# Performance work log

Hardware: AMD Instinct MI355X
Metric: run time of the kernel (lower is better)

## Reference

```python
import jax, jax.numpy as jnp
import numpy as np
import math


def _dct2_mat(N):
    # DCT-II matrix, norm=None convention of torch_dct: X[k] = 2*sum_n x[n]*cos(pi*(2n+1)*k/(2N))
    n = np.arange(N)
    k = n[:, None]
    C = 2.0 * np.cos(np.pi * (2 * n[None, :] + 1) * k / (2 * N))
    return jnp.asarray(C, dtype=jnp.float32)


def setup_inputs() -> dict:
    key = jax.random.key(0)
    k1, k2, k3 = jax.random.split(key, 3)
    B, H, W = 128, 256, 256
    thresh = int(H / (2 * math.sqrt(2)))  # 90
    x = jax.random.normal(k1, (B, 3, H, W), dtype=jnp.float32)
    w = jax.random.normal(k2, (1, thresh), dtype=jnp.float32) * 0.05
    b = jax.random.normal(k3, (1,), dtype=jnp.float32) * 0.05
    return {"x": x, "w": w, "b": b}


def reference(x, w, b):
    B, C, H, W = x.shape
    Ch = _dct2_mat(H)
    Cw = _dct2_mat(W)
    # dct_2d: DCT-II along last two dims
    xd = jnp.einsum('bchw,kw->bchk', x, Cw)
    xd = jnp.einsum('bchk,jh->bcjk', xd, Ch)
    xd = jax.lax.stop_gradient(xd)  # original does x.detach() inside get_fft_feature
    gray = 0.2989 * xd[:, 0] + 0.587 * xd[:, 1] + 0.114 * xd[:, 2]  # [B,H,W]
    F = jnp.fft.fft2(gray, axes=(-2, -1))
    re = F.real + 1e-8  # original adds epsilon to both real and imag parts
    im = F.imag + 1e-8
    mag = jnp.log(jnp.sqrt(re * re + im * im + 1e-10) + 1e-10)
    mag = jnp.fft.fftshift(mag, axes=(-2, -1))  # quadrant-swap `shift` == fftshift for even dims
    # radial binning (static integer radii, as in azimuthalAverage)
    yy, xx = np.indices([H, W])
    r = np.sqrt((xx - H / 2) ** 2 + (yy - W / 2) ** 2).astype(np.int32).ravel()
    nbins = int(r.max()) + 1
    nr = jnp.asarray(np.bincount(r, minlength=nbins).astype(np.float32))
    rj = jnp.asarray(r)
    tbin = jax.vmap(lambda m: jax.ops.segment_sum(m, rj, num_segments=nbins))(mag.reshape(B, -1))
    prof = tbin / (nr + 1e-10)  # [B, nbins]
    prof = prof[:, 1:-2]  # azimuthalAverage returns radial_prof[1:-2]
    mn = jnp.min(prof, axis=1, keepdims=True)
    mx = jnp.max(prof, axis=1, keepdims=True)
    out = (prof - mn) / (mx - mn)
    out = jnp.where(jnp.isnan(out), 0.0, out)
    thresh = w.shape[1]
    feat = out[:, -thresh:]  # [B, thresh]
    return feat @ w.T + b  # [B, 1]
```

## Files before the change

### kernel.cpp

```cpp
#include <hip/hip_runtime.h>
#include <math.h>

#define NBINS 182
#define NB 128

typedef unsigned short u16;
typedef __attribute__((ext_vector_type(8))) short short8;
typedef __attribute__((ext_vector_type(4))) float f32x4;

__device__ __forceinline__ u16 f2bf(float f) {
    union { float f; unsigned u; } v; v.f = f;
    unsigned r = v.u + 0x7FFF + ((v.u >> 16) & 1);
    return (u16)(r >> 16);
}
__device__ __forceinline__ float bf2f(u16 u) {
    union { unsigned u; float f; } v; v.u = ((unsigned)u) << 16;
    return v.f;
}
__device__ __forceinline__ short8 negbf(short8 v) {
    short8 r;
#pragma unroll
    for (int i = 0; i < 8; ++i) r[i] = v[i] ^ (short)0x8000;
    return r;
}

__device__ __forceinline__ int radial_bin(int dx, int dy) {
    int d2 = dx * dx + dy * dy;
    int bin = (int)sqrtf((float)d2);
    while ((bin + 1) * (bin + 1) <= d2) ++bin;
    while (bin * bin > d2) --bin;
    return bin;
}

__global__ __launch_bounds__(256) void prep(const float* __restrict__ x,
                                            u16* __restrict__ G,
                                            float* __restrict__ M_re,
                                            float* __restrict__ M_im,
                                            u16* __restrict__ A1,
                                            float* __restrict__ nrpart,
                                            float* __restrict__ tbin) {
    __shared__ double ctab[1024];
    __shared__ double stab[1024];
    __shared__ float s[NBINS];
    int blk = blockIdx.x;
    int t = threadIdx.x;

    if (blk < 256) {
        for (int i = t; i < 1024; i += 256) {
            double a = 3.14159265358979323846 * (double)i / 512.0;
            ctab[i] = cos(a);
            stab[i] = sin(a);
        }
        __syncthreads();
        int j = blk;
        int w = t;
        double re = 0.0, im = 0.0;
        int tw = 2 * w + 1;
        for (int k = 0; k < 256; ++k) {
            int e = (4 * j * k) & 1023;
            int m = (tw * k) & 1023;
            double cw = 2.0 * ctab[m];
            re += ctab[e] * cw;
            im -= stab[e] * cw;
        }
        M_re[j * 256 + w] = (float)re;
        M_im[j * 256 + w] = (float)im;
        A1[j * 256 + w] = f2bf((float)re);
        A1[(j + 256) * 256 + w] = f2bf((float)im);
    } else if (blk < 512) {
        int i = blk - 256;
        if (t < NBINS) s[t] = 0.0f;
        __syncthreads();
        int bin = radial_bin(t - 128, i - 128);
        atomicAdd(&s[bin], 1.0f);
        __syncthreads();
        if (t < NBINS) nrpart[i * NBINS + t] = s[t];
    } else if (blk < 544) {
        int idx = (blk - 512) * 256 + t;
        for (int i = idx; i < NB * NBINS; i += 32 * 256) tbin[i] = 0.0f;
    } else {
        int tid = (blk - 544) * 256 + t;
        for (int i = tid; i < 2097152; i += 262144) {
            int idx = i * 4;
            int b = idx >> 16;
            int rem = idx & 65535;
            const float* p = x + (size_t)b * 196608 + rem;
            float4 r = *(const float4*)p;
            float4 g = *(const float4*)(p + 65536);
            float4 bl = *(const float4*)(p + 131072);
            float g0 = 0.2989f * r.x + 0.587f * g.x + 0.114f * bl.x;
            float g1 = 0.2989f * r.y + 0.587f * g.y + 0.114f * bl.y;
            float g2 = 0.2989f * r.z + 0.587f * g.z + 0.114f * bl.z;
            float g3 = 0.2989f * r.w + 0.587f * g.w + 0.114f * bl.w;
            uint2 o;
            o.x = (unsigned)f2bf(g0) | ((unsigned)f2bf(g1) << 16);
            o.y = (unsigned)f2bf(g2) | ((unsigned)f2bf(g3) << 16);
            *(uint2*)(G + idx) = o;
        }
    }
}

__global__ __launch_bounds__(256) void s1(const u16* __restrict__ A1,
                                          const u16* __restrict__ G,
                                          u16* __restrict__ Tt_re,
                                          u16* __restrict__ Tt_im) {
    __shared__ u16 As[128 * 40];
    __shared__ u16 Bs[128 * 40];
    int b = blockIdx.z;
    int r0 = blockIdx.y * 128;
    int h0 = blockIdx.x * 128;
    int t = threadIdx.x;
    int lane = t & 63, wv = t >> 6;
    int wr = (wv >> 1) * 64;
    int wc = (wv & 1) * 64;
    int fr = lane & 15;
    int fk = (lane >> 4) << 3;

    f32x4 acc[4][4];
#pragma unroll
    for (int i = 0; i < 4; ++i)
#pragma unroll
        for (int j = 0; j < 4; ++j) acc[i][j] = (f32x4){0.f, 0.f, 0.f, 0.f};

    const u16* Ap = A1 + (size_t)r0 * 256;
    const u16* Gp = G + (size_t)b * 65536 + (size_t)h0 * 256;

    for (int kk = 0; kk < 256; kk += 32) {
#pragma unroll
        for (int c = t; c < 512; c += 256) {
            int row = c >> 2, off = (c & 3) << 3;
            *(uint4*)&As[row * 40 + off] =
                *(const uint4*)(Ap + (size_t)row * 256 + kk + off);
            *(uint4*)&Bs[row * 40 + off] =
                *(const uint4*)(Gp + (size_t)row * 256 + kk + off);
        }
        __syncthreads();
        short8 af[4], bfr[4];
#pragma unroll
        for (int i = 0; i < 4; ++i)
            af[i] = *(const short8*)&As[(wr + i * 16 + fr) * 40 + fk];
#pragma unroll
        for (int j = 0; j < 4; ++j)
            bfr[j] = *(const short8*)&Bs[(wc + j * 16 + fr) * 40 + fk];
#pragma unroll
        for (int i = 0; i < 4; ++i)
#pragma unroll
            for (int j = 0; j < 4; ++j)
                acc[i][j] = __builtin_amdgcn_mfma_f32_16x16x32_bf16(
                    af[i], bfr[j], acc[i][j], 0, 0, 0);
        __syncthreads();
    }

    u16* dst = ((r0 < 256) ? Tt_re : Tt_im) + (size_t)b * 65536
             + (size_t)(r0 & 255) * 256;
    int rq = (lane >> 4) << 2;
#pragma unroll
    for (int i = 0; i < 4; ++i)
#pragma unroll
        for (int j = 0; j < 4; ++j) {
            int col = h0 + wc + j * 16 + fr;
#pragma unroll
            for (int reg = 0; reg < 4; ++reg) {
                int row = wr + i * 16 + rq + reg;
                dst[(size_t)row * 256 + col] = f2bf(acc[i][j][reg]);
            }
        }
}

__global__ __launch_bounds__(256) void s2f(const u16* __restrict__ A1,
                                           const float* __restrict__ M_re,
                                           const u16* __restrict__ Tt_re,
                                           const u16* __restrict__ Tt_im,
                                           float* __restrict__ tbin) {
    __shared__ u16 Ar[64 * 40], Ai[64 * 40], Br[64 * 40], Bi[64 * 40];
    __shared__ float sbins[NBINS];
    __shared__ float sM[256];
    int blk = blockIdx.x;
    int t = threadIdx.x;

    if (blk >= 1024) {
        int b = blk - 1024;
        sM[t] = M_re[128 * 256 + t];
        __syncthreads();
        if (t > 128) return;
        const u16* pr = Tt_re + (size_t)b * 65536 + (size_t)t * 256;
        const u16* pi = Tt_im + (size_t)b * 65536 + (size_t)t * 256;
        float re = 0.0f, im = 0.0f;
        for (int h = 0; h < 256; h += 8) {
            uint4 vr = *(const uint4*)(pr + h);
            uint4 vi = *(const uint4*)(pi + h);
            unsigned wr[4] = {vr.x, vr.y, vr.z, vr.w};
            unsigned wi[4] = {vi.x, vi.y, vi.z, vi.w};
#pragma unroll
            for (int q = 0; q < 4; ++q) {
                re = fmaf(sM[h + 2 * q], bf2f((u16)(wr[q] & 0xffff)), re);
                re = fmaf(sM[h + 2 * q + 1], bf2f((u16)(wr[q] >> 16)), re);
                im = fmaf(sM[h + 2 * q], bf2f((u16)(wi[q] & 0xffff)), im);
                im = fmaf(sM[h + 2 * q + 1], bf2f((u16)(wi[q] >> 16)), im);
            }
        }
        re += 1e-8f; im += 1e-8f;
        float mag = logf(sqrtf(re * re + im * im + 1e-10f) + 1e-10f);
        float wj = (t == 0 || t == 128) ? 1.0f : 2.0f;
        int dx = (t < 128) ? t : t - 256;
        int bin = radial_bin(dx, -128);
        atomicAdd(&tbin[b * NBINS + bin], wj * mag);
        return;
    }

    int b = blk >> 3;
    int u0 = ((blk >> 2) & 1) * 64;
    int j0 = (blk & 3) * 64;
    int lane = t & 63, wv = t >> 6;
    int wu = (wv >> 1) * 32;
    int wj = (wv & 1) * 32;
    int fr = lane & 15;
    int fk = (lane >> 4) << 3;

    for (int i = t; i < NBINS; i += 256) sbins[i] = 0.0f;

    f32x4 accr[2][2], acci[2][2];
#pragma unroll
    for (int i = 0; i < 2; ++i)
#pragma unroll
        for (int j = 0; j < 2; ++j) {
            accr[i][j] = (f32x4){0.f, 0.f, 0.f, 0.f};
            acci[i][j] = (f32x4){0.f, 0.f, 0.f, 0.f};
        }

    const u16* Apr = A1 + (size_t)u0 * 256;
    const u16* Api = A1 + (size_t)(256 + u0) * 256;
    const u16* Tr = Tt_re + (size_t)b * 65536 + (size_t)j0 * 256;
    const u16* Ti = Tt_im + (size_t)b * 65536 + (size_t)j0 * 256;

    int lrow = t >> 2, loff = (t & 3) << 3;

    for (int kk = 0; kk < 256; kk += 32) {
        *(uint4*)&Ar[lrow * 40 + loff] =
            *(const uint4*)(Apr + (size_t)lrow * 256 + kk + loff);
        *(uint4*)&Ai[lrow * 40 + loff] =
            *(const uint4*)(Api + (size_t)lrow * 256 + kk + loff);
        *(uint4*)&Br[lrow * 40 + loff] =
            *(const uint4*)(Tr + (size_t)lrow * 256 + kk + loff);
        *(uint4*)&Bi[lrow * 40 + loff] =
            *(const uint4*)(Ti + (size_t)lrow * 256 + kk + loff);
        __syncthreads();
        short8 arf[2], aif[2], naif[2], brf[2], bif[2];
#pragma unroll
        for (int i = 0; i < 2; ++i) {
            arf[i] = *(const short8*)&Ar[(wu + i * 16 + fr) * 40 + fk];
            aif[i] = *(const short8*)&Ai[(wu + i * 16 + fr) * 40 + fk];
            naif[i] = negbf(aif[i]);
        }
#pragma unroll
        for (int j = 0; j < 2; ++j) {
            brf[j] = *(const short8*)&Br[(wj + j * 16 + fr) * 40 + fk];
            bif[j] = *(const short8*)&Bi[(wj + j * 16 + fr) * 40 + fk];
        }
#pragma unroll
        for (int i = 0; i < 2; ++i)
#pragma unroll
            for (int j = 0; j < 2; ++j) {
                accr[i][j] = __builtin_amdgcn_mfma_f32_16x16x32_bf16(
                    arf[i], brf[j], accr[i][j], 0, 0, 0);
                accr[i][j] = __builtin_amdgcn_mfma_f32_16x16x32_bf16(
                    naif[i], bif[j], accr[i][j], 0, 0, 0);
                acci[i][j] = __builtin_amdgcn_mfma_f32_16x16x32_bf16(
                    arf[i], bif[j], acci[i][j], 0, 0, 0);
                acci[i][j] = __builtin_amdgcn_mfma_f32_16x16x32_bf16(
                    aif[i], brf[j], acci[i][j], 0, 0, 0);
            }
        __syncthreads();
    }

    int rq = (lane >> 4) << 2;
#pragma unroll
    for (int i = 0; i < 2; ++i)
#pragma unroll
        for (int j = 0; j < 2; ++j) {
            int v = j0 + wj + j * 16 + fr;
            int dx = (v < 128) ? v : v - 256;
#pragma unroll
            for (int reg = 0; reg < 4; ++reg) {
                int u = u0 + wu + i * 16 + rq + reg;
                float wrow = (u == 0) ? 1.0f : 2.0f;
                int bin = radial_bin(dx, u);
                float re = accr[i][j][reg] + 1e-8f;
                float im = acci[i][j][reg] + 1e-8f;
                float mag = logf(sqrtf(re * re + im * im + 1e-10f) + 1e-10f);
                atomicAdd(&sbins[bin], wrow * mag);
            }
        }
    __syncthreads();
    for (int i = t; i < NBINS; i += 256)
        atomicAdd(&tbin[b * NBINS + i], sbins[i]);
}

__global__ __launch_bounds__(192) void finalize(const float* __restrict__ tbin,
                                                const float* __restrict__ nrpart,
                                                const float* __restrict__ w,
                                                const float* __restrict__ bias,
                                                float* __restrict__ out) {
    __shared__ float prof[NBINS];
    __shared__ float smn, smx, ssum;
    int b = blockIdx.x;
    int t = threadIdx.x;
    if (t < NBINS) {
        float nr = 0.0f;
        for (int i = 0; i < 256; ++i) nr += nrpart[i * NBINS + t];
        prof[t] = tbin[b * NBINS + t] / (nr + 1e-10f);
    }
    __syncthreads();
    if (t == 0) {
        float mn = prof[1], mx = prof[1];
        for (int i = 2; i <= 179; ++i) {
            float p = prof[i];
            mn = fminf(mn, p);
            mx = fmaxf(mx, p);
        }
        smn = mn; smx = mx; ssum = 0.0f;
    }
    __syncthreads();
    if (t < 90) {
        float denom = smx - smn;
        float v = (prof[90 + t] - smn) / denom;
        if (v != v) v = 0.0f;
        atomicAdd(&ssum, v * w[t]);
    }
    __syncthreads();
    if (t == 0) out[b] = ssum + bias[0];
}

extern "C" void kernel_launch(void* const* d_in, const int* in_sizes, int n_in,
                              void* d_out, int out_size, void* d_ws, size_t ws_size,
                              hipStream_t stream) {
    const float* x = (const float*)d_in[0];
    const float* w = (const float*)d_in[1];
    const float* bias = (const float*)d_in[2];
    float* out = (float*)d_out;

    float* M_re = (float*)d_ws;
    float* M_im = M_re + 65536;
    u16* A1 = (u16*)(M_im + 65536);
    u16* G = A1 + 131072;
    u16* Tt_re = G + (size_t)NB * 65536;
    u16* Tt_im = Tt_re + (size_t)NB * 65536;
    float* tbin = (float*)(Tt_im + (size_t)NB * 65536);
    float* nrpart = tbin + NB * NBINS;

    prep<<<1568, 256, 0, stream>>>(x, G, M_re, M_im, A1, nrpart, tbin);
    s1<<<dim3(2, 4, NB), 256, 0, stream>>>(A1, G, Tt_re, Tt_im);
    s2f<<<1152, 256, 0, stream>>>(A1, M_re, Tt_re, Tt_im, tbin);
    finalize<<<NB, 192, 0, stream>>>(tbin, nrpart, w, bias, out);
}
```

Before: 229.5 us.

## Exploit conjugate symmetry of real-input transform to halve first-stage GEMM

The first matmul stage now computes only rows 0..128 of the complex transform of the real gray image. The second stage reconstructs rows above 128 by mirroring (row 256-j) and flipping the sign of the imaginary part, so the s1 grid shrinks from 4 to 3 row-tiles. A small special block computes the lone row 128, and prep zeroes the matching imaginary row. This roughly halves first-stage MFMA work and Tt writes, at the cost of extra index logic, a sign-flip XOR in s2f loads and an unevenly sized extra block.

```diff
diff --git a/kernel.cpp b/kernel.cpp
--- a/kernel.cpp
+++ b/kernel.cpp
@@ -38,7 +38,8 @@
                                             float* __restrict__ M_im,
                                             u16* __restrict__ A1,
                                             float* __restrict__ nrpart,
-                                            float* __restrict__ tbin) {
+                                            float* __restrict__ tbin,
+                                            u16* __restrict__ Tt_im) {
     __shared__ double ctab[1024];
     __shared__ double stab[1024];
     __shared__ float s[NBINS];
@@ -78,6 +79,10 @@
     } else if (blk < 544) {
         int idx = (blk - 512) * 256 + t;
         for (int i = idx; i < NB * NBINS; i += 32 * 256) tbin[i] = 0.0f;
+        for (int i = idx; i < NB * 128; i += 32 * 256) {
+            int b = i >> 7, off = (i & 127) << 1;
+            *(unsigned*)(Tt_im + (size_t)b * 65536 + 128 * 256 + off) = 0u;
+        }
     } else {
         int tid = (blk - 544) * 256 + t;
         for (int i = tid; i < 2097152; i += 262144) {
@@ -104,12 +109,40 @@
                                           const u16* __restrict__ G,
                                           u16* __restrict__ Tt_re,
                                           u16* __restrict__ Tt_im) {
+    int b = blockIdx.z;
+    int t = threadIdx.x;
+
+    if (blockIdx.y == 2) {
+        int lane = t & 63, wv = t >> 6;
+        int fr = lane & 15;
+        int fk = (lane >> 4) << 3;
+        const u16* Ap = A1 + (size_t)(128 + fr) * 256;
+        const u16* Gb = G + (size_t)b * 65536;
+        int c0 = blockIdx.x * 128 + wv * 32;
+        f32x4 acc[2];
+        acc[0] = (f32x4){0.f, 0.f, 0.f, 0.f};
+        acc[1] = (f32x4){0.f, 0.f, 0.f, 0.f};
+        for (int kk = 0; kk < 256; kk += 32) {
+            short8 af = *(const short8*)(Ap + kk + fk);
+#pragma unroll
+            for (int sub = 0; sub < 2; ++sub) {
+                short8 bfv = *(const short8*)(Gb + (size_t)(c0 + sub * 16 + fr) * 256 + kk + fk);
+                acc[sub] = __builtin_amdgcn_mfma_f32_16x16x32_bf16(
+                    af, bfv, acc[sub], 0, 0, 0);
+            }
+        }
+        if ((lane >> 4) == 0) {
+            size_t base = (size_t)b * 65536 + 128 * 256;
+            Tt_re[base + c0 + lane] = f2bf(acc[0][0]);
+            Tt_re[base + c0 + 16 + lane] = f2bf(acc[1][0]);
+        }
+        return;
+    }
+
     __shared__ u16 As[128 * 40];
     __shared__ u16 Bs[128 * 40];
-    int b = blockIdx.z;
-    int r0 = blockIdx.y * 128;
+    int r0 = blockIdx.y * 256;
     int h0 = blockIdx.x * 128;
-    int t = threadIdx.x;
     int lane = t & 63, wv = t >> 6;
     int wr = (wv >> 1) * 64;
     int wc = (wv & 1) * 64;
@@ -151,8 +184,7 @@
         __syncthreads();
     }
 
-    u16* dst = ((r0 < 256) ? Tt_re : Tt_im) + (size_t)b * 65536
-             + (size_t)(r0 & 255) * 256;
+    u16* dst = ((r0 < 256) ? Tt_re : Tt_im) + (size_t)b * 65536;
     int rq = (lane >> 4) << 2;
 #pragma unroll
     for (int i = 0; i < 4; ++i)
@@ -230,20 +262,23 @@
 
     const u16* Apr = A1 + (size_t)u0 * 256;
     const u16* Api = A1 + (size_t)(256 + u0) * 256;
-    const u16* Tr = Tt_re + (size_t)b * 65536 + (size_t)j0 * 256;
-    const u16* Ti = Tt_im + (size_t)b * 65536 + (size_t)j0 * 256;
 
     int lrow = t >> 2, loff = (t & 3) << 3;
+    int jp = j0 + lrow;
+    int src = (jp <= 128) ? jp : 256 - jp;
+    unsigned imask = (jp > 128) ? 0x80008000u : 0u;
+    const u16* Trs = Tt_re + (size_t)b * 65536 + (size_t)src * 256;
+    const u16* Tis = Tt_im + (size_t)b * 65536 + (size_t)src * 256;
 
     for (int kk = 0; kk < 256; kk += 32) {
         *(uint4*)&Ar[lrow * 40 + loff] =
             *(const uint4*)(Apr + (size_t)lrow * 256 + kk + loff);
         *(uint4*)&Ai[lrow * 40 + loff] =
             *(const uint4*)(Api + (size_t)lrow * 256 + kk + loff);
-        *(uint4*)&Br[lrow * 40 + loff] =
-            *(const uint4*)(Tr + (size_t)lrow * 256 + kk + loff);
-        *(uint4*)&Bi[lrow * 40 + loff] =
-            *(const uint4*)(Ti + (size_t)lrow * 256 + kk + loff);
+        *(uint4*)&Br[lrow * 40 + loff] = *(const uint4*)(Trs + kk + loff);
+        uint4 vi = *(const uint4*)(Tis + kk + loff);
+        vi.x ^= imask; vi.y ^= imask; vi.z ^= imask; vi.w ^= imask;
+        *(uint4*)&Bi[lrow * 40 + loff] = vi;
         __syncthreads();
         short8 arf[2], aif[2], naif[2], brf[2], bif[2];
 #pragma unroll
@@ -348,8 +383,8 @@
     float* tbin = (float*)(Tt_im + (size_t)NB * 65536);
     float* nrpart = tbin + NB * NBINS;
 
-    prep<<<1568, 256, 0, stream>>>(x, G, M_re, M_im, A1, nrpart, tbin);
-    s1<<<dim3(2, 4, NB), 256, 0, stream>>>(A1, G, Tt_re, Tt_im);
+    prep<<<1568, 256, 0, stream>>>(x, G, M_re, M_im, A1, nrpart, tbin, Tt_im);
+    s1<<<dim3(2, 3, NB), 256, 0, stream>>>(A1, G, Tt_re, Tt_im);
     s2f<<<1152, 256, 0, stream>>>(A1, M_re, Tt_re, Tt_im, tbin);
     finalize<<<NB, 192, 0, stream>>>(tbin, nrpart, w, bias, out);
 }
```

Measured after the change: 223.9 us. -2.5%, faster.

## Fuse grayscale into first DFT stage, exploit Hermitian symmetry, merge finalize into s2f

Applied to the files above, without the earlier changes.

The grayscale conversion moves out of prep and into s1, which now reads x directly and builds bf16 tiles in shared memory. This removes the G intermediate buffer and one global round trip. s1 computes only rows 0..128 of the first-stage transform by using conjugate symmetry (real input), and s2f rebuilds rows above 128 by mirroring and sign-flipping the imaginary part. The finalize kernel is folded into s2f through a per-batch completion counter with a threadfence, so the last block for each batch computes the output. This cuts launches and memory traffic but adds atomic-counter synchronization and a more complex indexing scheme.

```diff
diff --git a/kernel.cpp b/kernel.cpp
--- a/kernel.cpp
+++ b/kernel.cpp
@@ -32,13 +32,13 @@
     return bin;
 }
 
-__global__ __launch_bounds__(256) void prep(const float* __restrict__ x,
-                                            u16* __restrict__ G,
-                                            float* __restrict__ M_re,
+__global__ __launch_bounds__(256) void prep(float* __restrict__ M_re,
                                             float* __restrict__ M_im,
                                             u16* __restrict__ A1,
                                             float* __restrict__ nrpart,
-                                            float* __restrict__ tbin) {
+                                            float* __restrict__ tbin,
+                                            u16* __restrict__ Tt_im,
+                                            unsigned* __restrict__ done) {
     __shared__ double ctab[1024];
     __shared__ double stab[1024];
     __shared__ float s[NBINS];
@@ -75,44 +75,31 @@
         atomicAdd(&s[bin], 1.0f);
         __syncthreads();
         if (t < NBINS) nrpart[i * NBINS + t] = s[t];
-    } else if (blk < 544) {
+    } else {
         int idx = (blk - 512) * 256 + t;
-        for (int i = idx; i < NB * NBINS; i += 32 * 256) tbin[i] = 0.0f;
-    } else {
-        int tid = (blk - 544) * 256 + t;
-        for (int i = tid; i < 2097152; i += 262144) {
-            int idx = i * 4;
-            int b = idx >> 16;
-            int rem = idx & 65535;
-            const float* p = x + (size_t)b * 196608 + rem;
-            float4 r = *(const float4*)p;
-            float4 g = *(const float4*)(p + 65536);
-            float4 bl = *(const float4*)(p + 131072);
-            float g0 = 0.2989f * r.x + 0.587f * g.x + 0.114f * bl.x;
-            float g1 = 0.2989f * r.y + 0.587f * g.y + 0.114f * bl.y;
-            float g2 = 0.2989f * r.z + 0.587f * g.z + 0.114f * bl.z;
-            float g3 = 0.2989f * r.w + 0.587f * g.w + 0.114f * bl.w;
-            uint2 o;
-            o.x = (unsigned)f2bf(g0) | ((unsigned)f2bf(g1) << 16);
-            o.y = (unsigned)f2bf(g2) | ((unsigned)f2bf(g3) << 16);
-            *(uint2*)(G + idx) = o;
-        }
-    }
-}
-
-__global__ __launch_bounds__(256) void s1(const u16* __restrict__ A1,
-                                          const u16* __restrict__ G,
+        for (int i = idx; i < NB * NBINS; i += 8192) tbin[i] = 0.0f;
+        for (int i = idx; i < NB * 128; i += 8192) {
+            int bb = i >> 7, off = (i & 127) << 1;
+            *(unsigned*)(Tt_im + (size_t)bb * 65536 + 128 * 256 + off) = 0u;
+        }
+        if (idx < NB) done[idx] = 0u;
+    }
+}
+
+__global__ __launch_bounds__(512) void s1(const u16* __restrict__ A1,
+                                          const float* __restrict__ x,
                                           u16* __restrict__ Tt_re,
                                           u16* __restrict__ Tt_im) {
-    __shared__ u16 As[128 * 40];
+    __shared__ u16 As[272 * 40];
     __shared__ u16 Bs[128 * 40];
     int b = blockIdx.z;
-    int r0 = blockIdx.y * 128;
     int h0 = blockIdx.x * 128;
     int t = threadIdx.x;
     int lane = t & 63, wv = t >> 6;
-    int wr = (wv >> 1) * 64;
-    int wc = (wv & 1) * 64;
+    int w4 = wv & 3;
+    int wr = (w4 >> 1) * 64;
+    int wc = (w4 & 1) * 64;
+    int aOff = (wv >= 4) ? 128 : 0;
     int fr = lane & 15;
     int fk = (lane >> 4) << 3;
 
@@ -121,24 +108,46 @@
     for (int i = 0; i < 4; ++i)
 #pragma unroll
         for (int j = 0; j < 4; ++j) acc[i][j] = (f32x4){0.f, 0.f, 0.f, 0.f};
-
-    const u16* Ap = A1 + (size_t)r0 * 256;
-    const u16* Gp = G + (size_t)b * 65536 + (size_t)h0 * 256;
+    f32x4 acc128 = (f32x4){0.f, 0.f, 0.f, 0.f};
+
+    int srow = t >> 2, swq = (t & 3) << 3;
+    const float* xp = x + (size_t)b * 196608 + (size_t)(h0 + srow) * 256 + swq;
 
     for (int kk = 0; kk < 256; kk += 32) {
-#pragma unroll
-        for (int c = t; c < 512; c += 256) {
+        for (int c = t; c < 1088; c += 512) {
             int row = c >> 2, off = (c & 3) << 3;
+            int src = (row < 128) ? row : ((row < 256) ? row + 128 : row - 128);
             *(uint4*)&As[row * 40 + off] =
-                *(const uint4*)(Ap + (size_t)row * 256 + kk + off);
-            *(uint4*)&Bs[row * 40 + off] =
-                *(const uint4*)(Gp + (size_t)row * 256 + kk + off);
+                *(const uint4*)(A1 + (size_t)src * 256 + kk + off);
+        }
+        {
+            const float* p = xp + kk;
+            float4 ra = *(const float4*)p;
+            float4 rb = *(const float4*)(p + 4);
+            float4 ga = *(const float4*)(p + 65536);
+            float4 gb = *(const float4*)(p + 65540);
+            float4 ba = *(const float4*)(p + 131072);
+            float4 bb = *(const float4*)(p + 131076);
+            float q0 = 0.2989f * ra.x + 0.587f * ga.x + 0.114f * ba.x;
+            float q1 = 0.2989f * ra.y + 0.587f * ga.y + 0.114f * ba.y;
+            float q2 = 0.2989f * ra.z + 0.587f * ga.z + 0.114f * ba.z;
+            float q3 = 0.2989f * ra.w + 0.587f * ga.w + 0.114f * ba.w;
+            float q4 = 0.2989f * rb.x + 0.587f * gb.x + 0.114f * bb.x;
+            float q5 = 0.2989f * rb.y + 0.587f * gb.y + 0.114f * bb.y;
+            float q6 = 0.2989f * rb.z + 0.587f * gb.z + 0.114f * bb.z;
+            float q7 = 0.2989f * rb.w + 0.587f * gb.w + 0.114f * bb.w;
+            uint4 o;
+            o.x = (unsigned)f2bf(q0) | ((unsigned)f2bf(q1) << 16);
+            o.y = (unsigned)f2bf(q2) | ((unsigned)f2bf(q3) << 16);
+            o.z = (unsigned)f2bf(q4) | ((unsigned)f2bf(q5) << 16);
+            o.w = (unsigned)f2bf(q6) | ((unsigned)f2bf(q7) << 16);
+            *(uint4*)&Bs[srow * 40 + swq] = o;
         }
         __syncthreads();
         short8 af[4], bfr[4];
 #pragma unroll
         for (int i = 0; i < 4; ++i)
-            af[i] = *(const short8*)&As[(wr + i * 16 + fr) * 40 + fk];
+            af[i] = *(const short8*)&As[(aOff + wr + i * 16 + fr) * 40 + fk];
 #pragma unroll
         for (int j = 0; j < 4; ++j)
             bfr[j] = *(const short8*)&Bs[(wc + j * 16 + fr) * 40 + fk];
@@ -148,11 +157,16 @@
             for (int j = 0; j < 4; ++j)
                 acc[i][j] = __builtin_amdgcn_mfma_f32_16x16x32_bf16(
                     af[i], bfr[j], acc[i][j], 0, 0, 0);
-        __syncthreads();
-    }
-
-    u16* dst = ((r0 < 256) ? Tt_re : Tt_im) + (size_t)b * 65536
-             + (size_t)(r0 & 255) * 256;
+        {
+            short8 a128 = *(const short8*)&As[(256 + fr) * 40 + fk];
+            short8 b128 = *(const short8*)&Bs[(wv * 16 + fr) * 40 + fk];
+            acc128 = __builtin_amdgcn_mfma_f32_16x16x32_bf16(
+                a128, b128, acc128, 0, 0, 0);
+        }
+        __syncthreads();
+    }
+
+    u16* dst = ((wv < 4) ? Tt_re : Tt_im) + (size_t)b * 65536;
     int rq = (lane >> 4) << 2;
 #pragma unroll
     for (int i = 0; i < 4; ++i)
@@ -165,170 +179,183 @@
                 dst[(size_t)row * 256 + col] = f2bf(acc[i][j][reg]);
             }
         }
+    if ((lane >> 4) == 0)
+        Tt_re[(size_t)b * 65536 + 128 * 256 + h0 + wv * 16 + fr] = f2bf(acc128[0]);
 }
 
 __global__ __launch_bounds__(256) void s2f(const u16* __restrict__ A1,
                                            const float* __restrict__ M_re,
                                            const u16* __restrict__ Tt_re,
                                            const u16* __restrict__ Tt_im,
-                                           float* __restrict__ tbin) {
+                                           float* __restrict__ tbin,
+                                           const float* __restrict__ nrpart,
+                                           const float* __restrict__ wgt,
+                                           const float* __restrict__ bias,
+                                           float* __restrict__ out,
+                                           unsigned* __restrict__ done) {
     __shared__ u16 Ar[64 * 40], Ai[64 * 40], Br[64 * 40], Bi[64 * 40];
     __shared__ float sbins[NBINS];
     __shared__ float sM[256];
+    __shared__ float prof[NBINS];
+    __shared__ float smn, smx, ssum;
+    __shared__ int sOld;
     int blk = blockIdx.x;
     int t = threadIdx.x;
+    int b;
 
     if (blk >= 1024) {
-        int b = blk - 1024;
+        b = blk - 1024;
         sM[t] = M_re[128 * 256 + t];
         __syncthreads();
-        if (t > 128) return;
-        const u16* pr = Tt_re + (size_t)b * 65536 + (size_t)t * 256;
-        const u16* pi = Tt_im + (size_t)b * 65536 + (size_t)t * 256;
-        float re = 0.0f, im = 0.0f;
-        for (int h = 0; h < 256; h += 8) {
-            uint4 vr = *(const uint4*)(pr + h);
-            uint4 vi = *(const uint4*)(pi + h);
-            unsigned wr[4] = {vr.x, vr.y, vr.z, vr.w};
-            unsigned wi[4] = {vi.x, vi.y, vi.z, vi.w};
-#pragma unroll
-            for (int q = 0; q < 4; ++q) {
-                re = fmaf(sM[h + 2 * q], bf2f((u16)(wr[q] & 0xffff)), re);
-                re = fmaf(sM[h + 2 * q + 1], bf2f((u16)(wr[q] >> 16)), re);
-                im = fmaf(sM[h + 2 * q], bf2f((u16)(wi[q] & 0xffff)), im);
-                im = fmaf(sM[h + 2 * q + 1], bf2f((u16)(wi[q] >> 16)), im);
-            }
-        }
-        re += 1e-8f; im += 1e-8f;
-        float mag = logf(sqrtf(re * re + im * im + 1e-10f) + 1e-10f);
-        float wj = (t == 0 || t == 128) ? 1.0f : 2.0f;
-        int dx = (t < 128) ? t : t - 256;
-        int bin = radial_bin(dx, -128);
-        atomicAdd(&tbin[b * NBINS + bin], wj * mag);
-        return;
-    }
-
-    int b = blk >> 3;
-    int u0 = ((blk >> 2) & 1) * 64;
-    int j0 = (blk & 3) * 64;
-    int lane = t & 63, wv = t >> 6;
-    int wu = (wv >> 1) * 32;
-    int wj = (wv & 1) * 32;
-    int fr = lane & 15;
-    int fk = (lane >> 4) << 3;
-
-    for (int i = t; i < NBINS; i += 256) sbins[i] = 0.0f;
-
-    f32x4 accr[2][2], acci[2][2];
-#pragma unroll
-    for (int i = 0; i < 2; ++i)
-#pragma unroll
-        for (int j = 0; j < 2; ++j) {
-            accr[i][j] = (f32x4){0.f, 0.f, 0.f, 0.f};
-            acci[i][j] = (f32x4){0.f, 0.f, 0.f, 0.f};
-        }
-
-    const u16* Apr = A1 + (size_t)u0 * 256;
-    const u16* Api = A1 + (size_t)(256 + u0) * 256;
-    const u16* Tr = Tt_re + (size_t)b * 65536 + (size_t)j0 * 256;
-    const u16* Ti = Tt_im + (size_t)b * 65536 + (size_t)j0 * 256;
-
-    int lrow = t >> 2, loff = (t & 3) << 3;
-
-    for (int kk = 0; kk < 256; kk += 32) {
-        *(uint4*)&Ar[lrow * 40 + loff] =
-            *(const uint4*)(Apr + (size_t)lrow * 256 + kk + loff);
-        *(uint4*)&Ai[lrow * 40 + loff] =
-            *(const uint4*)(Api + (size_t)lrow * 256 + kk + loff);
-        *(uint4*)&Br[lrow * 40 + loff] =
-            *(const uint4*)(Tr + (size_t)lrow * 256 + kk + loff);
-        *(uint4*)&Bi[lrow * 40 + loff] =
-            *(const uint4*)(Ti + (size_t)lrow * 256 + kk + loff);
-        __syncthreads();
-        short8 arf[2], aif[2], naif[2], brf[2], bif[2];
-#pragma unroll
-        for (int i = 0; i < 2; ++i) {
-            arf[i] = *(const short8*)&Ar[(wu + i * 16 + fr) * 40 + fk];
-            aif[i] = *(const short8*)&Ai[(wu + i * 16 + fr) * 40 + fk];
-            naif[i] = negbf(aif[i]);
-        }
-#pragma unroll
-        for (int j = 0; j < 2; ++j) {
-            brf[j] = *(const short8*)&Br[(wj + j * 16 + fr) * 40 + fk];
-            bif[j] = *(const short8*)&Bi[(wj + j * 16 + fr) * 40 + fk];
-        }
+        if (t <= 128) {
+            const u16* pr = Tt_re + (size_t)b * 65536 + (size_t)t * 256;
+            const u16* pi = Tt_im + (size_t)b * 65536 + (size_t)t * 256;
+            float re = 0.0f, im = 0.0f;
+            for (int h = 0; h < 256; h += 8) {
+                uint4 vr = *(const uint4*)(pr + h);
+                uint4 vi = *(const uint4*)(pi + h);
+                unsigned wr[4] = {vr.x, vr.y, vr.z, vr.w};
+                unsigned wi[4] = {vi.x, vi.y, vi.z, vi.w};
+#pragma unroll
+                for (int q = 0; q < 4; ++q) {
+                    re = fmaf(sM[h + 2 * q], bf2f((u16)(wr[q] & 0xffff)), re);
+                    re = fmaf(sM[h + 2 * q + 1], bf2f((u16)(wr[q] >> 16)), re);
+                    im = fmaf(sM[h + 2 * q], bf2f((u16)(wi[q] & 0xffff)), im);
+                    im = fmaf(sM[h + 2 * q + 1], bf2f((u16)(wi[q] >> 16)), im);
+                }
+            }
+            re += 1e-8f; im += 1e-8f;
+            float mag = logf(sqrtf(re * re + im * im + 1e-10f) + 1e-10f);
+            float wj = (t == 0 || t == 128) ? 1.0f : 2.0f;
+            int dx = (t < 128) ? t : t - 256;
+            int bin = radial_bin(dx, -128);
+            atomicAdd(&tbin[b * NBINS + bin], wj * mag);
+        }
+    } else {
+        b = blk >> 3;
+        int u0 = ((blk >> 2) & 1) * 64;
+        int j0 = (blk & 3) * 64;
+        int lane = t & 63, wv = t >> 6;
+        int wu = (wv >> 1) * 32;
+        int wj = (wv & 1) * 32;
+        int fr = lane & 15;
+        int fk = (lane >> 4) << 3;
+
+        for (int i = t; i < NBINS; i += 256) sbins[i] = 0.0f;
+
+        f32x4 accr[2][2], acci[2][2];
 #pragma unroll
         for (int i = 0; i < 2; ++i)
 #pragma unroll
             for (int j = 0; j < 2; ++j) {
-                accr[i][j] = __builtin_amdgcn_mfma_f32_16x16x32_bf16(
-                    arf[i], brf[j], accr[i][j], 0, 0, 0);
-                accr[i][j] = __builtin_amdgcn_mfma_f32_16x16x32_bf16(
-                    naif[i], bif[j], accr[i][j], 0, 0, 0);
-                acci[i][j] = __builtin_amdgcn_mfma_f32_16x16x32_bf16(
-                    arf[i], bif[j], acci[i][j], 0, 0, 0);
-                acci[i][j] = __builtin_amdgcn_mfma_f32_16x16x32_bf16(
-                    aif[i], brf[j], acci[i][j], 0, 0, 0);
-            }
-        __syncthreads();
-    }
-
-    int rq = (lane >> 4) << 2;
-#pragma unroll
-    for (int i = 0; i < 2; ++i)
-#pragma unroll
-        for (int j = 0; j < 2; ++j) {
-            int v = j0 + wj + j * 16 + fr;
-            int dx = (v < 128) ? v : v - 256;
-#pragma unroll
-            for (int reg = 0; reg < 4; ++reg) {
-                int u = u0 + wu + i * 16 + rq + reg;
-                float wrow = (u == 0) ? 1.0f : 2.0f;
-                int bin = radial_bin(dx, u);
-                float re = accr[i][j][reg] + 1e-8f;
-                float im = acci[i][j][reg] + 1e-8f;
-                float mag = logf(sqrtf(re * re + im * im + 1e-10f) + 1e-10f);
-                atomicAdd(&sbins[bin], wrow * mag);
-            }
-        }
-    __syncthreads();
-    for (int i = t; i < NBINS; i += 256)
-        atomicAdd(&tbin[b * NBINS + i], sbins[i]);
-}
-
-__global__ __launch_bounds__(192) void finalize(const float* __restrict__ tbin,
-                                                const float* __restrict__ nrpart,
-                                                const float* __restrict__ w,
-                                                const float* __restrict__ bias,
-                                                float* __restrict__ out) {
-    __shared__ float prof[NBINS];
-    __shared__ float smn, smx, ssum;
-    int b = blockIdx.x;
-    int t = threadIdx.x;
-    if (t < NBINS) {
-        float nr = 0.0f;
-        for (int i = 0; i < 256; ++i) nr += nrpart[i * NBINS + t];
-        prof[t] = tbin[b * NBINS + t] / (nr + 1e-10f);
-    }
+                accr[i][j] = (f32x4){0.f, 0.f, 0.f, 0.f};
+                acci[i][j] = (f32x4){0.f, 0.f, 0.f, 0.f};
+            }
+
+        const u16* Apr = A1 + (size_t)u0 * 256;
+        const u16* Api = A1 + (size_t)(256 + u0) * 256;
+
+        int lrow = t >> 2, loff = (t & 3) << 3;
+        int jp = j0 + lrow;
+        int src = (jp <= 128) ? jp : 256 - jp;
+        unsigned imask = (jp > 128) ? 0x80008000u : 0u;
+        const u16* Trs = Tt_re + (size_t)b * 65536 + (size_t)src * 256;
+        const u16* Tis = Tt_im + (size_t)b * 65536 + (size_t)src * 256;
+
+        for (int kk = 0; kk < 256; kk += 32) {
+            *(uint4*)&Ar[lrow * 40 + loff] =
+                *(const uint4*)(Apr + (size_t)lrow * 256 + kk + loff);
+            *(uint4*)&Ai[lrow * 40 + loff] =
+                *(const uint4*)(Api + (size_t)lrow * 256 + kk + loff);
+            *(uint4*)&Br[lrow * 40 + loff] = *(const uint4*)(Trs + kk + loff);
+            uint4 vi = *(const uint4*)(Tis + kk + loff);
+            vi.x ^= imask; vi.y ^= imask; vi.z ^= imask; vi.w ^= imask;
+            *(uint4*)&Bi[lrow * 40 + loff] = vi;
+            __syncthreads();
+            short8 arf[2], aif[2], naif[2], brf[2], bif[2];
+#pragma unroll
+            for (int i = 0; i < 2; ++i) {
+                arf[i] = *(const short8*)&Ar[(wu + i * 16 + fr) * 40 + fk];
+                aif[i] = *(const short8*)&Ai[(wu + i * 16 + fr) * 40 + fk];
+                naif[i] = negbf(aif[i]);
+            }
+#pragma unroll
+            for (int j = 0; j < 2; ++j) {
+                brf[j] = *(const short8*)&Br[(wj + j * 16 + fr) * 40 + fk];
+                bif[j] = *(const short8*)&Bi[(wj + j * 16 + fr) * 40 + fk];
+            }
+#pragma unroll
+            for (int i = 0; i < 2; ++i)
+#pragma unroll
+                for (int j = 0; j < 2; ++j) {
+                    accr[i][j] = __builtin_amdgcn_mfma_f32_16x16x32_bf16(
+                        arf[i], brf[j], accr[i][j], 0, 0, 0);
+                    accr[i][j] = __builtin_amdgcn_mfma_f32_16x16x32_bf16(
+                        naif[i], bif[j], accr[i][j], 0, 0, 0);
+                    acci[i][j] = __builtin_amdgcn_mfma_f32_16x16x32_bf16(
+                        arf[i], bif[j], acci[i][j], 0, 0, 0);
+                    acci[i][j] = __builtin_amdgcn_mfma_f32_16x16x32_bf16(
+                        aif[i], brf[j], acci[i][j], 0, 0, 0);
+                }
+            __syncthreads();
+        }
+
+        int rq = (lane >> 4) << 2;
+#pragma unroll
+        for (int i = 0; i < 2; ++i)
+#pragma unroll
+            for (int j = 0; j < 2; ++j) {
+                int v = j0 + wj + j * 16 + fr;
+                int dx = (v < 128) ? v : v - 256;
+#pragma unroll
+                for (int reg = 0; reg < 4; ++reg) {
+                    int u = u0 + wu + i * 16 + rq + reg;
+                    float wrow = (u == 0) ? 1.0f : 2.0f;
+                    int bin = radial_bin(dx, u);
+                    float re = accr[i][j][reg] + 1e-8f;
+                    float im = acci[i][j][reg] + 1e-8f;
+                    float mag = logf(sqrtf(re * re + im * im + 1e-10f) + 1e-10f);
+                    atomicAdd(&sbins[bin], wrow * mag);
+                }
+            }
+        __syncthreads();
+        for (int i = t; i < NBINS; i += 256)
+            atomicAdd(&tbin[b * NBINS + i], sbins[i]);
+    }
+
     __syncthreads();
     if (t == 0) {
-        float mn = prof[1], mx = prof[1];
-        for (int i = 2; i <= 179; ++i) {
-            float p = prof[i];
-            mn = fminf(mn, p);
-            mx = fmaxf(mx, p);
-        }
-        smn = mn; smx = mx; ssum = 0.0f;
+        __threadfence();
+        sOld = (int)atomicAdd(&done[b], 1u);
     }
     __syncthreads();
-    if (t < 90) {
-        float denom = smx - smn;
-        float v = (prof[90 + t] - smn) / denom;
-        if (v != v) v = 0.0f;
-        atomicAdd(&ssum, v * w[t]);
-    }
-    __syncthreads();
-    if (t == 0) out[b] = ssum + bias[0];
+    if (sOld == 8) {
+        if (t < NBINS) {
+            float nr = 0.0f;
+            for (int i = 0; i < 256; ++i) nr += nrpart[i * NBINS + t];
+            float tb = atomicAdd(&tbin[b * NBINS + t], 0.0f);
+            prof[t] = tb / (nr + 1e-10f);
+        }
+        __syncthreads();
+        if (t == 0) {
+            float mn = prof[1], mx = prof[1];
+            for (int i = 2; i <= 179; ++i) {
+                float p = prof[i];
+                mn = fminf(mn, p);
+                mx = fmaxf(mx, p);
+            }
+            smn = mn; smx = mx; ssum = 0.0f;
+        }
+        __syncthreads();
+        if (t < 90) {
+            float denom = smx - smn;
+            float v = (prof[90 + t] - smn) / denom;
+            if (v != v) v = 0.0f;
+            atomicAdd(&ssum, v * wgt[t]);
+        }
+        __syncthreads();
+        if (t == 0) out[b] = ssum + bias[0];
+    }
 }
 
 extern "C" void kernel_launch(void* const* d_in, const int* in_sizes, int n_in,
@@ -342,14 +369,14 @@
     float* M_re = (float*)d_ws;
     float* M_im = M_re + 65536;
     u16* A1 = (u16*)(M_im + 65536);
-    u16* G = A1 + 131072;
-    u16* Tt_re = G + (size_t)NB * 65536;
+    u16* Tt_re = A1 + 131072;
     u16* Tt_im = Tt_re + (size_t)NB * 65536;
     float* tbin = (float*)(Tt_im + (size_t)NB * 65536);
     float* nrpart = tbin + NB * NBINS;
-
-    prep<<<1568, 256, 0, stream>>>(x, G, M_re, M_im, A1, nrpart, tbin);
-    s1<<<dim3(2, 4, NB), 256, 0, stream>>>(A1, G, Tt_re, Tt_im);
-    s2f<<<1152, 256, 0, stream>>>(A1, M_re, Tt_re, Tt_im, tbin);
-    finalize<<<NB, 192, 0, stream>>>(tbin, nrpart, w, bias, out);
-}
+    unsigned* done = (unsigned*)(nrpart + 256 * NBINS);
+
+    prep<<<544, 256, 0, stream>>>(M_re, M_im, A1, nrpart, tbin, Tt_im, done);
+    s1<<<dim3(2, 1, NB), 512, 0, stream>>>(A1, x, Tt_re, Tt_im);
+    s2f<<<1152, 256, 0, stream>>>(A1, M_re, Tt_re, Tt_im, tbin,
+                                  nrpart, w, bias, out, done);
+}
```

Measured after the change: 241.4 us. 1.05x slower.
